# Kernel tuning notes

Measured on AMD Instinct MI355X. Metric: run time of the kernel, lower is better.

Reference implementation:

```python
import jax, jax.numpy as jnp
import numpy as np

B, T = 64, 500
N_EX, N_SK = 10000, 100
H, K = 128, 32


def setup_inputs() -> dict:
    key = jax.random.key(0)
    ks = jax.random.split(key, 32)
    g = lambda i, shape, s=0.05: (jax.random.normal(ks[i], shape, dtype=jnp.float32) * s)
    inp = {
        's_data': jax.random.randint(ks[0], (B, T), 0, N_SK),
        'a_data': jax.random.randint(ks[1], (B, T), 0, 2),
        'e_data': jax.random.randint(ks[2], (B, T), 0, N_EX),
        'at_data': jax.random.randint(ks[3], (B, T), 0, 100),
        'q_matrix': (jax.random.uniform(ks[4], (N_EX + 1, N_SK + 1)) < 0.05).astype(jnp.float32),
        's_embed_w': g(5, (N_SK + 1, H)),
        'a_embed_w': g(6, (2, H)),
        'e_embed_w': g(7, (N_EX + 1, H)),
        'W1': g(8, (H, 2 * H)), 'b1': jnp.zeros((H,), jnp.float32),
        'W2': g(9, (H, 3 * H)), 'b2': jnp.zeros((H,), jnp.float32),
        'W3': g(10, (H, 2 * H)), 'b3': jnp.zeros((H,), jnp.float32),
        'key_matrix': g(11, (K, H)),
        'gru_w_ih': g(12, (3 * H, H)), 'gru_w_hh': g(13, (3 * H, H)),
        'gru_b_ih': jnp.zeros((3 * H,), jnp.float32), 'gru_b_hh': jnp.zeros((3 * H,), jnp.float32),
        'Wg': g(14, (H, 2 * H)), 'bg': jnp.zeros((H,), jnp.float32),
        'Wgg': g(15, (H, 2 * H)), 'bgg': jnp.zeros((H,), jnp.float32),
        'Wf': g(16, (H, 2 * H)), 'bf': jnp.zeros((H,), jnp.float32),
        'Wp': g(17, (1, 3 * H)), 'bp': jnp.zeros((1,), jnp.float32),
        'Wp1': g(18, (1, 3 * H)), 'bp1': jnp.zeros((1,), jnp.float32),
        'h0': g(19, (H,)),           # xavier init of GRU initial state (shared across batch)
        'm0': g(20, (K, H)),         # xavier init of memory h_pre (shared across batch)
    }
    return inp


def reference(s_data, a_data, e_data, at_data, q_matrix, s_embed_w, a_embed_w, e_embed_w,
              W1, b1, W2, b2, W3, b3, key_matrix, gru_w_ih, gru_w_hh, gru_b_ih, gru_b_hh,
              Wg, bg, Wgg, bgg, Wf, bf, Wp, bp, Wp1, bp1, h0, m0):
    # eval mode: dropout = identity
    Bv, Tv = a_data.shape
    lin = lambda x, W, b: x @ W.T + b
    # ---- embedding (n_exercise > 0 branch) ----
    rel = q_matrix[e_data]                              # [B,T,S+1]
    ssum = rel.sum(-1, keepdims=True)
    ssum = jnp.where(ssum == 0, 1.0, ssum)
    s_emb = jnp.einsum('bts,sh->bth', rel, s_embed_w) / ssum
    e_emb = e_embed_w[e_data]
    a_emb = a_embed_w[a_data]
    se_data = jax.nn.relu(lin(jnp.concatenate([s_emb, e_emb], -1), W1, b1))
    se_learning = jax.nn.relu(lin(jnp.concatenate([s_emb, e_emb, a_emb], -1), W2, b2))
    e_learning = jax.nn.relu(lin(jnp.concatenate([e_emb, a_emb], -1), W3, b3))
    # ---- GRU over e_learning ----
    gx = jnp.einsum('bth,gh->btg', e_learning, gru_w_ih) + gru_b_ih  # [B,T,3H]
    def gru_step(h, gxt):
        gh = h @ gru_w_hh.T + gru_b_hh
        xr, xz, xn = jnp.split(gxt, 3, -1)
        hr, hz, hn = jnp.split(gh, 3, -1)
        r = jax.nn.sigmoid(xr + hr)
        z = jax.nn.sigmoid(xz + hz)
        n = jnp.tanh(xn + r * hn)
        hn2 = (1 - z) * n + z * h
        return hn2, hn2
    _, gru_out = jax.lax.scan(gru_step, jnp.broadcast_to(h0, (Bv, h0.shape[0])), jnp.swapaxes(gx, 0, 1))
    out = jnp.swapaxes(gru_out, 0, 1)[:, :-1]           # [B,T-1,H]
    # ---- key-value memory scan ----
    Wall = jnp.einsum('bth,kh->btk', se_data, key_matrix)  # attention weights (unnormalized)
    h_pre0 = jnp.broadcast_to(m0, (Bv,) + m0.shape)        # [B,K,H]
    ht0 = jnp.einsum('bk,bkh->bh', Wall[:, 0], h_pre0)
    xs = (jnp.swapaxes(Wall[:, :-1], 0, 1),
          jnp.swapaxes(Wall[:, 1:], 0, 1),
          jnp.swapaxes(se_learning[:, :-1], 0, 1))
    def step(carry, x):
        h_pre, ht_pre = carry
        w, w_next, learning = x
        hl = jnp.concatenate([ht_pre, learning], -1)
        gain = jnp.tanh(hl @ Wg.T + bg)
        gate = jax.nn.sigmoid(hl @ Wgg.T + bgg)
        LG = gate * gain                                  # [B,H]
        LG_t = w[:, :, None] * LG[:, None, :]             # [B,K,H] write
        gam = jax.nn.sigmoid(jnp.concatenate([h_pre, jnp.broadcast_to(LG[:, None, :], h_pre.shape)], -1) @ Wf.T + bf)
        h = gam * h_pre + LG_t
        ht = jnp.einsum('bk,bkh->bh', w_next, h)          # read at t+1
        return (h, ht), ht
    _, hts = jax.lax.scan(step, (h_pre0, ht0), xs)
    out1 = jnp.swapaxes(hts, 0, 1)                        # [B,T-1,H]
    sg = jax.lax.stop_gradient
    res = jax.nn.sigmoid(jnp.concatenate([out, sg(out1), e_emb[:, 1:]], -1) @ Wp.T + bp)[..., 0]
    res1 = jax.nn.sigmoid(jnp.concatenate([sg(out), out1, se_data[:, 1:]], -1) @ Wp1.T + bp1)[..., 0]
    pred = jnp.zeros((Bv, Tv), res.dtype).at[:, 1:].set(res * res1)
    return pred
```

## Files before the change

kernel.cpp:

```cpp
#include <hip/hip_runtime.h>

#define TT 500
typedef __attribute__((ext_vector_type(8))) short short8v;
typedef __attribute__((ext_vector_type(4))) short short4v;
typedef __attribute__((ext_vector_type(4))) float float4v;
typedef unsigned short ushort;

__device__ __forceinline__ ushort f2bf(float f) {
  union { float f; unsigned u; } v; v.f = f;
  unsigned r = v.u + 0x7FFFu + ((v.u >> 16) & 1u);
  return (ushort)(r >> 16);
}
__device__ __forceinline__ ushort f2bfr(float f) {
  union { float f; unsigned u; } v; v.f = f;
  return (ushort)((v.u + 0x8000u) >> 16);
}
__device__ __forceinline__ float bf2f(ushort u) {
  union { unsigned u; float f; } v; v.u = ((unsigned)u) << 16;
  return v.f;
}
__device__ __forceinline__ float sigm(float x) {
  return __builtin_amdgcn_rcpf(1.f + __builtin_amdgcn_exp2f(-1.44269504088896341f * x));
}
__device__ __forceinline__ float tanh_f(float x) {
  return 1.f - 2.f * __builtin_amdgcn_rcpf(1.f + __builtin_amdgcn_exp2f(2.88539008177792682f * x));
}
__device__ __forceinline__ void bar_lds() {
  asm volatile("s_waitcnt lgkmcnt(0)\ns_barrier" ::: "memory");
}
template <int CTRL>
__device__ __forceinline__ float dppadd(float v) {
  int a = __builtin_amdgcn_update_dpp(0, __builtin_bit_cast(int, v), CTRL, 0xF, 0xF, true);
  return v + __builtin_bit_cast(float, a);
}
__device__ __forceinline__ float rsum16(float v) {
  v = dppadd<0xB1>(v);
  v = dppadd<0x4E>(v);
  v = dppadd<0x141>(v);
  v = dppadd<0x140>(v);
  return v;
}
#define MFMA __builtin_amdgcn_mfma_f32_16x16x32_bf16

__global__ __launch_bounds__(256) void conv_k(
    const float* __restrict__ W1, const float* __restrict__ W2,
    const float* __restrict__ W3, const float* __restrict__ Wih,
    const float* __restrict__ key, const float* __restrict__ Wg,
    const float* __restrict__ Wgg, ushort* __restrict__ wts)
{
  int idx = blockIdx.x * 256 + threadIdx.x;
  if (idx >= 200704) return;
  float v;
  if (idx < 32768)       v = W1[idx];
  else if (idx < 81920)  v = W2[idx - 32768];
  else if (idx < 114688) v = W3[idx - 81920];
  else if (idx < 163840) v = Wih[idx - 114688];
  else if (idx < 167936) v = key[idx - 163840];
  else {
    int j = idx - 167936, o = j >> 7, k = j & 127;
    v = (o < 128) ? Wg[o * 256 + 128 + k] : Wgg[(o - 128) * 256 + 128 + k];
  }
  wts[idx] = f2bf(v);
}

__global__ __launch_bounds__(256) void ph_gather_k(
    const int* __restrict__ a_data, const int* __restrict__ e_data,
    const float* __restrict__ qm, const float* __restrict__ semb,
    const float* __restrict__ aemb, const float* __restrict__ eemb,
    ushort* __restrict__ Xg)
{
  const int tid = threadIdx.x;
  const int tok = tid >> 4, l16 = tid & 15;
  const int gt = blockIdx.x * 16 + tok;
  const int e = e_data[gt], a = a_data[gt];
  const float* qrow = qm + (size_t)e * 101;
  float qv[7];
#pragma unroll
  for (int i = 0; i < 7; ++i) {
    int s = l16 + 16 * i;
    qv[i] = (s < 101) ? qrow[s] : 0.f;
  }
  const float* sbase = semb + l16 * 8;
  float4v acc0 = {0,0,0,0}, acc1 = {0,0,0,0};
  float cnt = 0.f;
#pragma unroll
  for (int i = 0; i < 7; ++i) {
    unsigned long long bal = __ballot(qv[i] != 0.f);
    unsigned m = (unsigned)((bal >> (tid & 48)) & 0xFFFFull);
    cnt += (float)__popc(m);
    while (m) {
      int s = 16 * i + __builtin_ctz(m);
      m &= m - 1;
      acc0 += *(const float4v*)(sbase + s * 128);
      acc1 += *(const float4v*)(sbase + s * 128 + 4);
    }
  }
  float inv = 1.f / fmaxf(cnt, 1.f);
  ushort* xr = Xg + (size_t)gt * 384 + l16 * 8;
  const float* ee = eemb + (size_t)e * 128 + l16 * 8;
  const float* ae = aemb + a * 128 + l16 * 8;
  short4v p0, p1;
#pragma unroll
  for (int r = 0; r < 4; ++r) { p0[r] = (short)f2bf(acc0[r] * inv); p1[r] = (short)f2bf(acc1[r] * inv); }
  *(short4v*)(xr) = p0;
  *(short4v*)(xr + 4) = p1;
#pragma unroll
  for (int r = 0; r < 8; ++r) { xr[128 + r] = f2bf(ee[r]); xr[256 + r] = f2bf(ae[r]); }
}

#define XS 424
#define SS 648

__global__ __launch_bounds__(256, 2) void ph_gemm_k(
    const float* __restrict__ b1, const float* __restrict__ b2,
    const float* __restrict__ b3, const float* __restrict__ bih,
    const float* __restrict__ bg, const float* __restrict__ bgg,
    const float* __restrict__ Wp, const float* __restrict__ bp,
    const float* __restrict__ Wp1, const float* __restrict__ bp1,
    const ushort* __restrict__ wts,
    ushort* __restrict__ gxb, ushort* __restrict__ xgx,
    float* __restrict__ wallb, float* __restrict__ c1b, float* __restrict__ c2b)
{
  __shared__ __align__(16) ushort sbuf[27136];
  ushort* Xl = sbuf;
  ushort* Yl = sbuf + 13568;
  ushort* St = sbuf;
  const int tid = threadIdx.x;
  const int b = blockIdx.x >> 4, chunk = blockIdx.x & 15;
  const int t0 = chunk * 32;
  const int NT = (TT - t0 < 32) ? (TT - t0) : 32;
  const ushort* w1b  = wts;
  const ushort* w2b  = wts + 32768;
  const ushort* w3b  = wts + 81920;
  const ushort* wihb = wts + 114688;
  const ushort* keyb = wts + 163840;
  const ushort* wgb  = wts + 167936;

#pragma unroll
  for (int pass = 0; pass < 2; ++pass) {
    const int tok = (tid >> 4) + pass * 16, sg = tid & 15;
    const int tsrc = (tok < NT) ? tok : (NT - 1);
    size_t gt = (size_t)b * TT + t0 + tsrc;
#pragma unroll
    for (int p = 0; p < 3; ++p)
      *(short8v*)(Xl + tok * XS + sg * 24 + p * 8) = *(const short8v*)(gxb + gt * 384 + sg * 24 + p * 8);
  }
  __syncthreads();

  const int w = tid >> 6, l = tid & 63, jj = l & 15, seg = l >> 4;

  if (tid < 32) {
    int tau = tid;
    if (tau < NT) {
      const ushort* xr = Xl + tau * XS + 128;
      const float* wv = Wp + 256;
      float a0 = bp[0], a1 = 0.f, a2 = 0.f, a3 = 0.f;
      for (int j = 0; j < 128; j += 4) {
        a0 = fmaf(wv[j],     bf2f(xr[j]),     a0);
        a1 = fmaf(wv[j + 1], bf2f(xr[j + 1]), a1);
        a2 = fmaf(wv[j + 2], bf2f(xr[j + 2]), a2);
        a3 = fmaf(wv[j + 3], bf2f(xr[j + 3]), a3);
      }
      c1b[b * TT + t0 + tau] = (a0 + a1) + (a2 + a3);
    }
  }

  short8v axA[12], axB[12];
#pragma unroll
  for (int i = 0; i < 12; ++i) {
    axA[i] = *(short8v*)(Xl + jj * XS + i * 32 + seg * 8);
    axB[i] = *(short8v*)(Xl + (16 + jj) * XS + i * 32 + seg * 8);
  }

  for (int T = w; T < 24; T += 4) {
    float4v dA = {0,0,0,0}, dB = {0,0,0,0};
    float bv;
    if (T < 8) {
      const ushort* Bp = w1b + (T * 16 + jj) * 256 + seg * 8;
      bv = b1[T * 16 + jj];
#pragma unroll
      for (int k = 0; k < 8; ++k) {
        short8v bw = *(const short8v*)(Bp + k * 32);
        dA = MFMA(axA[k], bw, dA, 0, 0, 0);
        dB = MFMA(axB[k], bw, dB, 0, 0, 0);
      }
    } else if (T < 16) {
      const ushort* Bp = w2b + ((T - 8) * 16 + jj) * 384 + seg * 8;
      bv = b2[(T - 8) * 16 + jj];
#pragma unroll
      for (int k = 0; k < 12; ++k) {
        short8v bw = *(const short8v*)(Bp + k * 32);
        dA = MFMA(axA[k], bw, dA, 0, 0, 0);
        dB = MFMA(axB[k], bw, dB, 0, 0, 0);
      }
    } else {
      const ushort* Bp = w3b + ((T - 16) * 16 + jj) * 256 + seg * 8;
      bv = b3[(T - 16) * 16 + jj];
#pragma unroll
      for (int k = 0; k < 8; ++k) {
        short8v bw = *(const short8v*)(Bp + k * 32);
        dA = MFMA(axA[4 + k], bw, dA, 0, 0, 0);
        dB = MFMA(axB[4 + k], bw, dB, 0, 0, 0);
      }
    }
#pragma unroll
    for (int r = 0; r < 4; ++r) {
      float yA = dA[r] + bv, yB = dB[r] + bv;
      Yl[(seg * 4 + r) * XS + T * 16 + jj]      = f2bf(yA > 0.f ? yA : 0.f);
      Yl[(16 + seg * 4 + r) * XS + T * 16 + jj] = f2bf(yB > 0.f ? yB : 0.f);
    }
  }
  __syncthreads();

  short8v ayA[12], ayB[12];
#pragma unroll
  for (int i = 0; i < 12; ++i) {
    ayA[i] = *(short8v*)(Yl + jj * XS + i * 32 + seg * 8);
    ayB[i] = *(short8v*)(Yl + (16 + jj) * XS + i * 32 + seg * 8);
  }

  if (tid >= 32 && tid < 64) {
    int tau = tid - 32;
    if (tau < NT) {
      const ushort* xr = Yl + tau * XS;
      const float* wv = Wp1 + 256;
      float a0 = bp1[0], a1 = 0.f, a2 = 0.f, a3 = 0.f;
      for (int j = 0; j < 128; j += 4) {
        a0 = fmaf(wv[j],     bf2f(xr[j]),     a0);
        a1 = fmaf(wv[j + 1], bf2f(xr[j + 1]), a1);
        a2 = fmaf(wv[j + 2], bf2f(xr[j + 2]), a2);
        a3 = fmaf(wv[j + 3], bf2f(xr[j + 3]), a3);
      }
      c2b[b * TT + t0 + tau] = (a0 + a1) + (a2 + a3);
    }
  }
  __syncthreads();

  for (int T = w; T < 42; T += 4) {
    const ushort* Bp; int ai;
    if (T < 24)      { Bp = wihb + (T * 16 + jj) * 128 + seg * 8;        ai = 8; }
    else if (T < 40) { Bp = wgb  + ((T - 24) * 16 + jj) * 128 + seg * 8; ai = 4; }
    else             { Bp = keyb + ((T - 40) * 16 + jj) * 128 + seg * 8; ai = 0; }
    float4v dA = {0,0,0,0}, dB = {0,0,0,0};
#pragma unroll
    for (int k = 0; k < 4; ++k) {
      short8v bw = *(const short8v*)(Bp + k * 32);
      dA = MFMA(ayA[ai + k], bw, dA, 0, 0, 0);
      dB = MFMA(ayB[ai + k], bw, dB, 0, 0, 0);
    }
    if (T < 40) {
      float bv = (T < 24) ? bih[T * 16 + jj]
               : (T < 32) ? bg[(T - 24) * 16 + jj] : bgg[(T - 32) * 16 + jj];
      int col = (T < 24) ? (T * 16 + jj) : (384 + (T - 24) * 16 + jj);
#pragma unroll
      for (int r = 0; r < 4; ++r) {
        St[(seg * 4 + r) * SS + col]      = f2bf(dA[r] + bv);
        St[(16 + seg * 4 + r) * SS + col] = f2bf(dB[r] + bv);
      }
    } else {
#pragma unroll
      for (int r = 0; r < 4; ++r) {
        int tokA = seg * 4 + r, tokB = 16 + seg * 4 + r;
        if (tokA < NT)
          wallb[((size_t)(b * TT + t0 + tokA)) * 32 + (T - 40) * 16 + jj] = dA[r];
        if (tokB < NT)
          wallb[((size_t)(b * TT + t0 + tokB)) * 32 + (T - 40) * 16 + jj] = dB[r];
      }
    }
  }
  __syncthreads();

#pragma unroll
  for (int pass = 0; pass < 2; ++pass) {
    const int tok = (tid >> 4) + pass * 16, sg = tid & 15;
    if (tok < NT) {
      size_t gt = (size_t)b * TT + t0 + tok;
#pragma unroll
      for (int p = 0; p < 3; ++p)
        *(short8v*)(gxb + gt * 384 + sg * 24 + p * 8) = *(short8v*)(St + tok * SS + sg * 24 + p * 8);
#pragma unroll
      for (int p = 0; p < 2; ++p)
        *(short8v*)(xgx + gt * 256 + sg * 16 + p * 8) = *(short8v*)(St + tok * SS + 384 + sg * 16 + p * 8);
    }
  }
}

__global__ __launch_bounds__(512) void scan_k(
    const float* __restrict__ Wf, const float* __restrict__ bf_,
    const float* __restrict__ Wg, const float* __restrict__ Wgg,
    const float* __restrict__ Whh, const float* __restrict__ bhh,
    const float* __restrict__ h0v, const float* __restrict__ m0,
    const ushort* __restrict__ gxb, const ushort* __restrict__ xgx,
    const float* __restrict__ wallb,
    ushort* __restrict__ htsm, ushort* __restrict__ htsg)
{
  const int tid = threadIdx.x;
  const int w = tid >> 6, l = tid & 63, jj = l & 15, seg = l >> 4;
  const int n0 = w * 16 + seg * 4;

  if (blockIdx.x < 64) {
    const int b = blockIdx.x;
    __shared__ __align__(16) ushort h_bf[32 * 128];
    __shared__ __align__(16) ushort htb[128];
    __shared__ __align__(16) ushort LGb[128];

    short8v afrA[4], aggA[4], aggB[4], alg[4];
#pragma unroll
    for (int ks = 0; ks < 4; ++ks) {
      const float* sA = Wf  + (w * 16 + jj) * 256 + ks * 32 + seg * 8;
      const float* sB = Wg  + (w * 16 + jj) * 256 + ks * 32 + seg * 8;
      const float* sC = Wgg + (w * 16 + jj) * 256 + ks * 32 + seg * 8;
      const float* sD = Wf  + (w * 16 + jj) * 256 + 128 + ks * 32 + seg * 8;
      short8v a, bb, c, d;
#pragma unroll
      for (int j = 0; j < 8; ++j) {
        a[j] = (short)f2bf(sA[j]); bb[j] = (short)f2bf(sB[j]);
        c[j] = (short)f2bf(sC[j]); d[j] = (short)f2bf(sD[j]);
      }
      afrA[ks] = a; aggA[ks] = bb; aggB[ks] = c; alg[ks] = d;
    }
    const float4v bf4 = *(const float4v*)(bf_ + n0);

    float hreg[2][4];
#pragma unroll
    for (int nt = 0; nt < 2; ++nt) {
      int k = nt * 16 + jj;
      float4v m = *(const float4v*)(m0 + k * 128 + n0);
#pragma unroll
      for (int r = 0; r < 4; ++r) hreg[nt][r] = m[r];
      int p = ((n0 >> 3) + k) & 15;
      short4v pk;
#pragma unroll
      for (int r = 0; r < 4; ++r) pk[r] = (short)f2bf(hreg[nt][r]);
      *(short4v*)(h_bf + k * 128 + p * 8 + (n0 & 7)) = pk;
    }
    const float* wl = wallb + (size_t)b * TT * 32;
    const ushort* xgp = xgx + (size_t)b * TT * 256;
    float wv0 = wl[jj], wv1 = wl[16 + jj];
    float wn0 = wl[32 + jj], wn1 = wl[48 + jj];
    short4v xcg  = *(const short4v*)(xgp + n0);
    short4v xcgg = *(const short4v*)(xgp + 128 + n0);
    short4v xng  = *(const short4v*)(xgp + 256 + n0);
    short4v xngg = *(const short4v*)(xgp + 384 + n0);
    {
      float4v htp;
#pragma unroll
      for (int r = 0; r < 4; ++r)
        htp[r] = rsum16(wv0 * hreg[0][r] + wv1 * hreg[1][r]);
      if (jj == 0) {
        short4v hp;
#pragma unroll
        for (int r = 0; r < 4; ++r) hp[r] = (short)f2bf(htp[r]);
        *(short4v*)(htb + n0) = hp;
      }
    }
    __syncthreads();

    for (int t = 0; t < TT - 1; ++t) {
      int tw = (t + 2 <= TT - 1) ? (t + 2) : (TT - 1);
      float wf0 = wl[tw * 32 + jj], wf1 = wl[tw * 32 + 16 + jj];
      short4v xfg  = *(const short4v*)(xgp + (size_t)tw * 256 + n0);
      short4v xfgg = *(const short4v*)(xgp + (size_t)tw * 256 + 128 + n0);

      short8v hb[4];
#pragma unroll
      for (int ks = 0; ks < 4; ++ks)
        hb[ks] = *(short8v*)(htb + ks * 32 + seg * 8);

      float4v xg4, xgg4;
#pragma unroll
      for (int r = 0; r < 4; ++r) { xg4[r] = bf2f((ushort)xcg[r]); xgg4[r] = bf2f((ushort)xcgg[r]); }
      float4v dg0 = xg4, dg1 = {0,0,0,0}, gg0 = xgg4, gg1 = {0,0,0,0};
      dg0 = MFMA(aggA[0], hb[0], dg0, 0, 0, 0);
      dg0 = MFMA(aggA[1], hb[1], dg0, 0, 0, 0);
      dg1 = MFMA(aggA[2], hb[2], dg1, 0, 0, 0);
      dg1 = MFMA(aggA[3], hb[3], dg1, 0, 0, 0);
      gg0 = MFMA(aggB[0], hb[0], gg0, 0, 0, 0);
      gg0 = MFMA(aggB[1], hb[1], gg0, 0, 0, 0);
      gg1 = MFMA(aggB[2], hb[2], gg1, 0, 0, 0);
      gg1 = MFMA(aggB[3], hb[3], gg1, 0, 0, 0);

      float lgv[4];
#pragma unroll
      for (int r = 0; r < 4; ++r)
        lgv[r] = tanh_f(dg0[r] + dg1[r]) * sigm(gg0[r] + gg1[r]);
      if (jj == 0) {
        short4v lp;
#pragma unroll
        for (int r = 0; r < 4; ++r) lp[r] = (short)f2bfr(lgv[r]);
        *(short4v*)(LGb + n0) = lp;
      }

      short8v bv0[4], bv1[4];
#pragma unroll
      for (int ks = 0; ks < 4; ++ks) {
        int g = ks * 4 + seg;
        bv0[ks] = *(short8v*)(h_bf + jj * 128 + ((g + jj) & 15) * 8);
        bv1[ks] = *(short8v*)(h_bf + (16 + jj) * 128 + ((g + 16 + jj) & 15) * 8);
      }
      float4v a0A = {0,0,0,0}, a0B = {0,0,0,0}, a1A = {0,0,0,0}, a1B = {0,0,0,0};
      a0A = MFMA(afrA[0], bv0[0], a0A, 0, 0, 0);
      a0A = MFMA(afrA[1], bv0[1], a0A, 0, 0, 0);
      a0B = MFMA(afrA[2], bv0[2], a0B, 0, 0, 0);
      a0B = MFMA(afrA[3], bv0[3], a0B, 0, 0, 0);
      a1A = MFMA(afrA[0], bv1[0], a1A, 0, 0, 0);
      a1A = MFMA(afrA[1], bv1[1], a1A, 0, 0, 0);
      a1B = MFMA(afrA[2], bv1[2], a1B, 0, 0, 0);
      a1B = MFMA(afrA[3], bv1[3], a1B, 0, 0, 0);
      bar_lds();

      short8v lb[4];
#pragma unroll
      for (int ks = 0; ks < 4; ++ks)
        lb[ks] = *(short8v*)(LGb + ks * 32 + seg * 8);
      float4v dl0 = bf4, dl1 = {0,0,0,0};
      dl0 = MFMA(alg[0], lb[0], dl0, 0, 0, 0);
      dl0 = MFMA(alg[1], lb[1], dl0, 0, 0, 0);
      dl1 = MFMA(alg[2], lb[2], dl1, 0, 0, 0);
      dl1 = MFMA(alg[3], lb[3], dl1, 0, 0, 0);

      float4v htp = {0,0,0,0};
#pragma unroll
      for (int nt = 0; nt < 2; ++nt) {
        float wvv = nt ? wv1 : wv0;
        float wnn = nt ? wn1 : wn0;
#pragma unroll
        for (int r = 0; r < 4; ++r) {
          float a = nt ? (a1A[r] + a1B[r]) : (a0A[r] + a0B[r]);
          float gam = sigm(a + dl0[r] + dl1[r]);
          float hn = fmaf(gam, hreg[nt][r], wvv * lgv[r]);
          hreg[nt][r] = hn;
          htp[r] = fmaf(wnn, hn, htp[r]);
        }
        int k = nt * 16 + jj;
        int p = ((n0 >> 3) + k) & 15;
        short4v pk;
#pragma unroll
        for (int r = 0; r < 4; ++r) pk[r] = (short)f2bfr(hreg[nt][r]);
        *(short4v*)(h_bf + k * 128 + p * 8 + (n0 & 7)) = pk;
      }
#pragma unroll
      for (int r = 0; r < 4; ++r) htp[r] = rsum16(htp[r]);
      if (jj == 0) {
        short4v hp;
#pragma unroll
        for (int r = 0; r < 4; ++r) hp[r] = (short)f2bfr(htp[r]);
        *(short4v*)(htb + n0) = hp;
        *(short4v*)(htsm + ((size_t)b * TT + t) * 128 + n0) = hp;
      }
      wv0 = wn0; wv1 = wn1; wn0 = wf0; wn1 = wf1;
      xcg = xng; xcgg = xngg; xng = xfg; xngg = xfgg;
      bar_lds();
    }
  } else {
    const int b = blockIdx.x - 64;
    __shared__ __align__(16) ushort hb2[2][128];

    short8v wfr[3][4];
    float4v bfr[3];
#pragma unroll
    for (int i = 0; i < 3; ++i) {
      int Mt = w + i * 8;
#pragma unroll
      for (int ks = 0; ks < 4; ++ks) {
        const float* src = Whh + (Mt * 16 + jj) * 128 + ks * 32 + seg * 8;
        short8v tv;
#pragma unroll
        for (int j = 0; j < 8; ++j) tv[j] = (short)f2bf(src[j]);
        wfr[i][ks] = tv;
      }
      bfr[i] = *(const float4v*)(bhh + Mt * 16 + seg * 4);
    }
    const ushort* gpb = gxb + (size_t)b * TT * 384;
    float4v hj4 = *(const float4v*)(h0v + n0);
    if (jj == 0) {
      short4v hp;
#pragma unroll
      for (int r = 0; r < 4; ++r) hp[r] = (short)f2bf(hj4[r]);
      *(short4v*)(&hb2[0][n0]) = hp;
    }
    short4v xr_c = *(const short4v*)(gpb + n0);
    short4v xz_c = *(const short4v*)(gpb + 128 + n0);
    short4v xn_c = *(const short4v*)(gpb + 256 + n0);
    short4v xr_n = *(const short4v*)(gpb + 384 + n0);
    short4v xz_n = *(const short4v*)(gpb + 512 + n0);
    short4v xn_n = *(const short4v*)(gpb + 640 + n0);
    __syncthreads();

    for (int t = 0; t < TT - 1; ++t) {
      int tf = (t + 2 < TT - 1) ? (t + 2) : (TT - 2);
      const ushort* gf = gpb + (size_t)tf * 384;
      short4v xr_f = *(const short4v*)(gf + n0);
      short4v xz_f = *(const short4v*)(gf + 128 + n0);
      short4v xn_f = *(const short4v*)(gf + 256 + n0);

      const ushort* hsrc = hb2[t & 1];
      short8v bfrg[4];
#pragma unroll
      for (int ks = 0; ks < 4; ++ks)
        bfrg[ks] = *(short8v*)(hsrc + ks * 32 + seg * 8);

      float4v a0A = bfr[0], a1A = bfr[1], a2A = bfr[2];
      float4v a0B = {0,0,0,0}, a1B = {0,0,0,0}, a2B = {0,0,0,0};
      a0A = MFMA(wfr[0][0], bfrg[0], a0A, 0, 0, 0);
      a0A = MFMA(wfr[0][1], bfrg[1], a0A, 0, 0, 0);
      a0B = MFMA(wfr[0][2], bfrg[2], a0B, 0, 0, 0);
      a0B = MFMA(wfr[0][3], bfrg[3], a0B, 0, 0, 0);
      a1A = MFMA(wfr[1][0], bfrg[0], a1A, 0, 0, 0);
      a1A = MFMA(wfr[1][1], bfrg[1], a1A, 0, 0, 0);
      a1B = MFMA(wfr[1][2], bfrg[2], a1B, 0, 0, 0);
      a1B = MFMA(wfr[1][3], bfrg[3], a1B, 0, 0, 0);
      a2A = MFMA(wfr[2][0], bfrg[0], a2A, 0, 0, 0);
      a2A = MFMA(wfr[2][1], bfrg[1], a2A, 0, 0, 0);
      a2B = MFMA(wfr[2][2], bfrg[2], a2B, 0, 0, 0);
      a2B = MFMA(wfr[2][3], bfrg[3], a2B, 0, 0, 0);

      ushort* hdst = (ushort*)hb2[(t + 1) & 1];
      short4v hp;
#pragma unroll
      for (int r = 0; r < 4; ++r) {
        float rr = sigm(bf2f((ushort)xr_c[r]) + a0A[r] + a0B[r]);
        float zz = sigm(bf2f((ushort)xz_c[r]) + a1A[r] + a1B[r]);
        float nn = tanh_f(bf2f((ushort)xn_c[r]) + rr * (a2A[r] + a2B[r]));
        hj4[r] = fmaf(1.f - zz, nn, zz * hj4[r]);
        hp[r] = (short)f2bfr(hj4[r]);
      }
      if (jj == 0) {
        *(short4v*)(hdst + n0) = hp;
        *(short4v*)(htsg + ((size_t)b * TT + t) * 128 + n0) = hp;
      }
      xr_c = xr_n; xz_c = xz_n; xn_c = xn_n;
      xr_n = xr_f; xz_n = xz_f; xn_n = xn_f;
      bar_lds();
    }
  }
}

__global__ __launch_bounds__(256) void combine_k(
    const ushort* __restrict__ htsg, const ushort* __restrict__ htsm,
    const float* __restrict__ c1b, const float* __restrict__ c2b,
    const float* __restrict__ Wp, const float* __restrict__ Wp1,
    float* __restrict__ out)
{
  const int b = blockIdx.x;
  const int wv = threadIdx.x >> 6;
  const int lane = threadIdx.x & 63;
  const float w0 = Wp[lane], w1 = Wp[64 + lane], w2 = Wp[128 + lane], w3 = Wp[192 + lane];
  const float v0 = Wp1[lane], v1 = Wp1[64 + lane], v2 = Wp1[128 + lane], v3 = Wp1[192 + lane];
  if (threadIdx.x == 0) out[(size_t)b * TT] = 0.f;
  for (int tau = wv; tau < TT - 1; tau += 4) {
    size_t base = ((size_t)b * TT + tau) * 128;
    float hg0 = bf2f(htsg[base + lane]), hg1 = bf2f(htsg[base + 64 + lane]);
    float hm0 = bf2f(htsm[base + lane]), hm1 = bf2f(htsm[base + 64 + lane]);
    float qa = hg0 * w0 + hg1 * w1 + hm0 * w2 + hm1 * w3;
    float qb = hg0 * v0 + hg1 * v1 + hm0 * v2 + hm1 * v3;
#pragma unroll
    for (int m = 1; m < 64; m <<= 1) {
      qa += __shfl_xor(qa, m, 64);
      qb += __shfl_xor(qb, m, 64);
    }
    if (lane == 0) {
      size_t idx = (size_t)b * TT + tau + 1;
      out[idx] = sigm(qa + c1b[idx]) * sigm(qb + c2b[idx]);
    }
  }
}

extern "C" void kernel_launch(void* const* d_in, const int* in_sizes, int n_in,
                              void* d_out, int out_size, void* d_ws, size_t ws_size,
                              hipStream_t stream) {
  (void)in_sizes; (void)n_in; (void)out_size; (void)ws_size;
  const int* a_data = (const int*)d_in[1];
  const int* e_data = (const int*)d_in[2];
  const float* qm   = (const float*)d_in[4];
  const float* semb = (const float*)d_in[5];
  const float* aemb = (const float*)d_in[6];
  const float* eemb = (const float*)d_in[7];
  const float* W1 = (const float*)d_in[8];   const float* b1 = (const float*)d_in[9];
  const float* W2 = (const float*)d_in[10];  const float* b2 = (const float*)d_in[11];
  const float* W3 = (const float*)d_in[12];  const float* b3 = (const float*)d_in[13];
  const float* key = (const float*)d_in[14];
  const float* Wih = (const float*)d_in[15]; const float* Whh = (const float*)d_in[16];
  const float* bih = (const float*)d_in[17]; const float* bhh = (const float*)d_in[18];
  const float* Wg  = (const float*)d_in[19]; const float* bg  = (const float*)d_in[20];
  const float* Wgg = (const float*)d_in[21]; const float* bgg = (const float*)d_in[22];
  const float* Wf  = (const float*)d_in[23]; const float* bf_ = (const float*)d_in[24];
  const float* Wp  = (const float*)d_in[25]; const float* bp  = (const float*)d_in[26];
  const float* Wp1 = (const float*)d_in[27]; const float* bp1 = (const float*)d_in[28];
  const float* h0v = (const float*)d_in[29]; const float* m0  = (const float*)d_in[30];

  char* ws = (char*)d_ws;
  ushort* gxb  = (ushort*)(ws + 0);
  ushort* xgx  = (ushort*)(ws + 24576000);
  float* wallb = (float*)(ws + 40960000);
  ushort* htsm = (ushort*)(ws + 45056000);
  ushort* htsg = (ushort*)(ws + 53248000);
  float* c1b   = (float*)(ws + 61440000);
  float* c2b   = (float*)(ws + 61568000);
  ushort* wts  = (ushort*)(ws + 61696000);
  float* out = (float*)d_out;

  conv_k<<<dim3(784), dim3(256), 0, stream>>>(W1, W2, W3, Wih, key, Wg, Wgg, wts);
  ph_gather_k<<<dim3(2000), dim3(256), 0, stream>>>(
      a_data, e_data, qm, semb, aemb, eemb, gxb);
  ph_gemm_k<<<dim3(1024), dim3(256), 0, stream>>>(
      b1, b2, b3, bih, bg, bgg, Wp, bp, Wp1, bp1, wts,
      gxb, xgx, wallb, c1b, c2b);
  scan_k<<<dim3(128), dim3(512), 0, stream>>>(
      Wf, bf_, Wg, Wgg, Whh, bhh, h0v, m0, gxb, xgx, wallb, htsm, htsg);
  combine_k<<<dim3(64), dim3(256), 0, stream>>>(
      htsg, htsm, c1b, c2b, Wp, Wp1, out);
}
```

Before: 949.9 us.

## Fuse gather, projection GEMM and scans into one persistent kernel with flags

Merges the gather, projection GEMM and both recurrent scan kernels into a single launch. Blocks 0-127 run the sequential scans and spin on per-(chunk,batch) flags, while the remaining 1024 blocks gather embeddings, run the GEMMs for 32-token chunks, and set a release flag when each chunk is written. The scans can then start before all projections finish, overlapping the serial recurrence with the parallel precompute and removing the launch gaps and the gxb round trip from the gather stage. The risk is that it relies on scan blocks and producer blocks being co-resident and on forward progress, and the producer blocks now use 512 threads with halved per-warp tile loops.

Result: faster. 917.1 us (-3.5%).

```diff
diff --git a/kernel.cpp b/kernel.cpp
--- a/kernel.cpp
+++ b/kernel.cpp
@@ -39,6 +39,11 @@
   v = dppadd<0x141>(v);
   v = dppadd<0x140>(v);
   return v;
+}
+__device__ __forceinline__ void wait_flag(int* f) {
+  while (__hip_atomic_load(f, __ATOMIC_RELAXED, __HIP_MEMORY_SCOPE_AGENT) == 0)
+    __builtin_amdgcn_s_sleep(8);
+  __builtin_amdgcn_fence(__ATOMIC_ACQUIRE, "agent");
 }
 #define MFMA __builtin_amdgcn_mfma_f32_16x16x32_bf16
 
@@ -63,246 +68,38 @@
   wts[idx] = f2bf(v);
 }
 
-__global__ __launch_bounds__(256) void ph_gather_k(
+#define XS 424
+#define SS 648
+
+__global__ __launch_bounds__(512) void mega_k(
     const int* __restrict__ a_data, const int* __restrict__ e_data,
     const float* __restrict__ qm, const float* __restrict__ semb,
     const float* __restrict__ aemb, const float* __restrict__ eemb,
-    ushort* __restrict__ Xg)
-{
-  const int tid = threadIdx.x;
-  const int tok = tid >> 4, l16 = tid & 15;
-  const int gt = blockIdx.x * 16 + tok;
-  const int e = e_data[gt], a = a_data[gt];
-  const float* qrow = qm + (size_t)e * 101;
-  float qv[7];
-#pragma unroll
-  for (int i = 0; i < 7; ++i) {
-    int s = l16 + 16 * i;
-    qv[i] = (s < 101) ? qrow[s] : 0.f;
-  }
-  const float* sbase = semb + l16 * 8;
-  float4v acc0 = {0,0,0,0}, acc1 = {0,0,0,0};
-  float cnt = 0.f;
-#pragma unroll
-  for (int i = 0; i < 7; ++i) {
-    unsigned long long bal = __ballot(qv[i] != 0.f);
-    unsigned m = (unsigned)((bal >> (tid & 48)) & 0xFFFFull);
-    cnt += (float)__popc(m);
-    while (m) {
-      int s = 16 * i + __builtin_ctz(m);
-      m &= m - 1;
-      acc0 += *(const float4v*)(sbase + s * 128);
-      acc1 += *(const float4v*)(sbase + s * 128 + 4);
-    }
-  }
-  float inv = 1.f / fmaxf(cnt, 1.f);
-  ushort* xr = Xg + (size_t)gt * 384 + l16 * 8;
-  const float* ee = eemb + (size_t)e * 128 + l16 * 8;
-  const float* ae = aemb + a * 128 + l16 * 8;
-  short4v p0, p1;
-#pragma unroll
-  for (int r = 0; r < 4; ++r) { p0[r] = (short)f2bf(acc0[r] * inv); p1[r] = (short)f2bf(acc1[r] * inv); }
-  *(short4v*)(xr) = p0;
-  *(short4v*)(xr + 4) = p1;
-#pragma unroll
-  for (int r = 0; r < 8; ++r) { xr[128 + r] = f2bf(ee[r]); xr[256 + r] = f2bf(ae[r]); }
-}
-
-#define XS 424
-#define SS 648
-
-__global__ __launch_bounds__(256, 2) void ph_gemm_k(
     const float* __restrict__ b1, const float* __restrict__ b2,
     const float* __restrict__ b3, const float* __restrict__ bih,
     const float* __restrict__ bg, const float* __restrict__ bgg,
     const float* __restrict__ Wp, const float* __restrict__ bp,
     const float* __restrict__ Wp1, const float* __restrict__ bp1,
     const ushort* __restrict__ wts,
-    ushort* __restrict__ gxb, ushort* __restrict__ xgx,
-    float* __restrict__ wallb, float* __restrict__ c1b, float* __restrict__ c2b)
-{
-  __shared__ __align__(16) ushort sbuf[27136];
-  ushort* Xl = sbuf;
-  ushort* Yl = sbuf + 13568;
-  ushort* St = sbuf;
-  const int tid = threadIdx.x;
-  const int b = blockIdx.x >> 4, chunk = blockIdx.x & 15;
-  const int t0 = chunk * 32;
-  const int NT = (TT - t0 < 32) ? (TT - t0) : 32;
-  const ushort* w1b  = wts;
-  const ushort* w2b  = wts + 32768;
-  const ushort* w3b  = wts + 81920;
-  const ushort* wihb = wts + 114688;
-  const ushort* keyb = wts + 163840;
-  const ushort* wgb  = wts + 167936;
-
-#pragma unroll
-  for (int pass = 0; pass < 2; ++pass) {
-    const int tok = (tid >> 4) + pass * 16, sg = tid & 15;
-    const int tsrc = (tok < NT) ? tok : (NT - 1);
-    size_t gt = (size_t)b * TT + t0 + tsrc;
-#pragma unroll
-    for (int p = 0; p < 3; ++p)
-      *(short8v*)(Xl + tok * XS + sg * 24 + p * 8) = *(const short8v*)(gxb + gt * 384 + sg * 24 + p * 8);
-  }
-  __syncthreads();
-
-  const int w = tid >> 6, l = tid & 63, jj = l & 15, seg = l >> 4;
-
-  if (tid < 32) {
-    int tau = tid;
-    if (tau < NT) {
-      const ushort* xr = Xl + tau * XS + 128;
-      const float* wv = Wp + 256;
-      float a0 = bp[0], a1 = 0.f, a2 = 0.f, a3 = 0.f;
-      for (int j = 0; j < 128; j += 4) {
-        a0 = fmaf(wv[j],     bf2f(xr[j]),     a0);
-        a1 = fmaf(wv[j + 1], bf2f(xr[j + 1]), a1);
-        a2 = fmaf(wv[j + 2], bf2f(xr[j + 2]), a2);
-        a3 = fmaf(wv[j + 3], bf2f(xr[j + 3]), a3);
-      }
-      c1b[b * TT + t0 + tau] = (a0 + a1) + (a2 + a3);
-    }
-  }
-
-  short8v axA[12], axB[12];
-#pragma unroll
-  for (int i = 0; i < 12; ++i) {
-    axA[i] = *(short8v*)(Xl + jj * XS + i * 32 + seg * 8);
-    axB[i] = *(short8v*)(Xl + (16 + jj) * XS + i * 32 + seg * 8);
-  }
-
-  for (int T = w; T < 24; T += 4) {
-    float4v dA = {0,0,0,0}, dB = {0,0,0,0};
-    float bv;
-    if (T < 8) {
-      const ushort* Bp = w1b + (T * 16 + jj) * 256 + seg * 8;
-      bv = b1[T * 16 + jj];
-#pragma unroll
-      for (int k = 0; k < 8; ++k) {
-        short8v bw = *(const short8v*)(Bp + k * 32);
-        dA = MFMA(axA[k], bw, dA, 0, 0, 0);
-        dB = MFMA(axB[k], bw, dB, 0, 0, 0);
-      }
-    } else if (T < 16) {
-      const ushort* Bp = w2b + ((T - 8) * 16 + jj) * 384 + seg * 8;
-      bv = b2[(T - 8) * 16 + jj];
-#pragma unroll
-      for (int k = 0; k < 12; ++k) {
-        short8v bw = *(const short8v*)(Bp + k * 32);
-        dA = MFMA(axA[k], bw, dA, 0, 0, 0);
-        dB = MFMA(axB[k], bw, dB, 0, 0, 0);
-      }
-    } else {
-      const ushort* Bp = w3b + ((T - 16) * 16 + jj) * 256 + seg * 8;
-      bv = b3[(T - 16) * 16 + jj];
-#pragma unroll
-      for (int k = 0; k < 8; ++k) {
-        short8v bw = *(const short8v*)(Bp + k * 32);
-        dA = MFMA(axA[4 + k], bw, dA, 0, 0, 0);
-        dB = MFMA(axB[4 + k], bw, dB, 0, 0, 0);
-      }
-    }
-#pragma unroll
-    for (int r = 0; r < 4; ++r) {
-      float yA = dA[r] + bv, yB = dB[r] + bv;
-      Yl[(seg * 4 + r) * XS + T * 16 + jj]      = f2bf(yA > 0.f ? yA : 0.f);
-      Yl[(16 + seg * 4 + r) * XS + T * 16 + jj] = f2bf(yB > 0.f ? yB : 0.f);
-    }
-  }
-  __syncthreads();
-
-  short8v ayA[12], ayB[12];
-#pragma unroll
-  for (int i = 0; i < 12; ++i) {
-    ayA[i] = *(short8v*)(Yl + jj * XS + i * 32 + seg * 8);
-    ayB[i] = *(short8v*)(Yl + (16 + jj) * XS + i * 32 + seg * 8);
-  }
-
-  if (tid >= 32 && tid < 64) {
-    int tau = tid - 32;
-    if (tau < NT) {
-      const ushort* xr = Yl + tau * XS;
-      const float* wv = Wp1 + 256;
-      float a0 = bp1[0], a1 = 0.f, a2 = 0.f, a3 = 0.f;
-      for (int j = 0; j < 128; j += 4) {
-        a0 = fmaf(wv[j],     bf2f(xr[j]),     a0);
-        a1 = fmaf(wv[j + 1], bf2f(xr[j + 1]), a1);
-        a2 = fmaf(wv[j + 2], bf2f(xr[j + 2]), a2);
-        a3 = fmaf(wv[j + 3], bf2f(xr[j + 3]), a3);
-      }
-      c2b[b * TT + t0 + tau] = (a0 + a1) + (a2 + a3);
-    }
-  }
-  __syncthreads();
-
-  for (int T = w; T < 42; T += 4) {
-    const ushort* Bp; int ai;
-    if (T < 24)      { Bp = wihb + (T * 16 + jj) * 128 + seg * 8;        ai = 8; }
-    else if (T < 40) { Bp = wgb  + ((T - 24) * 16 + jj) * 128 + seg * 8; ai = 4; }
-    else             { Bp = keyb + ((T - 40) * 16 + jj) * 128 + seg * 8; ai = 0; }
-    float4v dA = {0,0,0,0}, dB = {0,0,0,0};
-#pragma unroll
-    for (int k = 0; k < 4; ++k) {
-      short8v bw = *(const short8v*)(Bp + k * 32);
-      dA = MFMA(ayA[ai + k], bw, dA, 0, 0, 0);
-      dB = MFMA(ayB[ai + k], bw, dB, 0, 0, 0);
-    }
-    if (T < 40) {
-      float bv = (T < 24) ? bih[T * 16 + jj]
-               : (T < 32) ? bg[(T - 24) * 16 + jj] : bgg[(T - 32) * 16 + jj];
-      int col = (T < 24) ? (T * 16 + jj) : (384 + (T - 24) * 16 + jj);
-#pragma unroll
-      for (int r = 0; r < 4; ++r) {
-        St[(seg * 4 + r) * SS + col]      = f2bf(dA[r] + bv);
-        St[(16 + seg * 4 + r) * SS + col] = f2bf(dB[r] + bv);
-      }
-    } else {
-#pragma unroll
-      for (int r = 0; r < 4; ++r) {
-        int tokA = seg * 4 + r, tokB = 16 + seg * 4 + r;
-        if (tokA < NT)
-          wallb[((size_t)(b * TT + t0 + tokA)) * 32 + (T - 40) * 16 + jj] = dA[r];
-        if (tokB < NT)
-          wallb[((size_t)(b * TT + t0 + tokB)) * 32 + (T - 40) * 16 + jj] = dB[r];
-      }
-    }
-  }
-  __syncthreads();
-
-#pragma unroll
-  for (int pass = 0; pass < 2; ++pass) {
-    const int tok = (tid >> 4) + pass * 16, sg = tid & 15;
-    if (tok < NT) {
-      size_t gt = (size_t)b * TT + t0 + tok;
-#pragma unroll
-      for (int p = 0; p < 3; ++p)
-        *(short8v*)(gxb + gt * 384 + sg * 24 + p * 8) = *(short8v*)(St + tok * SS + sg * 24 + p * 8);
-#pragma unroll
-      for (int p = 0; p < 2; ++p)
-        *(short8v*)(xgx + gt * 256 + sg * 16 + p * 8) = *(short8v*)(St + tok * SS + 384 + sg * 16 + p * 8);
-    }
-  }
-}
-
-__global__ __launch_bounds__(512) void scan_k(
     const float* __restrict__ Wf, const float* __restrict__ bf_,
     const float* __restrict__ Wg, const float* __restrict__ Wgg,
     const float* __restrict__ Whh, const float* __restrict__ bhh,
     const float* __restrict__ h0v, const float* __restrict__ m0,
-    const ushort* __restrict__ gxb, const ushort* __restrict__ xgx,
-    const float* __restrict__ wallb,
-    ushort* __restrict__ htsm, ushort* __restrict__ htsg)
+    ushort* __restrict__ gxb, ushort* __restrict__ xgx,
+    float* __restrict__ wallb, float* __restrict__ c1b, float* __restrict__ c2b,
+    ushort* __restrict__ htsm, ushort* __restrict__ htsg,
+    int* __restrict__ flags)
 {
+  __shared__ __align__(16) ushort pool[27136];
   const int tid = threadIdx.x;
   const int w = tid >> 6, l = tid & 63, jj = l & 15, seg = l >> 4;
   const int n0 = w * 16 + seg * 4;
 
   if (blockIdx.x < 64) {
     const int b = blockIdx.x;
-    __shared__ __align__(16) ushort h_bf[32 * 128];
-    __shared__ __align__(16) ushort htb[128];
-    __shared__ __align__(16) ushort LGb[128];
+    ushort* h_bf = pool;
+    ushort* htb  = pool + 4096;
+    ushort* LGb  = pool + 4224;
 
     short8v afrA[4], aggA[4], aggB[4], alg[4];
 #pragma unroll
@@ -334,6 +131,7 @@
       for (int r = 0; r < 4; ++r) pk[r] = (short)f2bf(hreg[nt][r]);
       *(short4v*)(h_bf + k * 128 + p * 8 + (n0 & 7)) = pk;
     }
+    wait_flag(flags + b);
     const float* wl = wallb + (size_t)b * TT * 32;
     const ushort* xgp = xgx + (size_t)b * TT * 256;
     float wv0 = wl[jj], wv1 = wl[16 + jj];
@@ -358,6 +156,7 @@
 
     for (int t = 0; t < TT - 1; ++t) {
       int tw = (t + 2 <= TT - 1) ? (t + 2) : (TT - 1);
+      if ((tw & 31) == 0) wait_flag(flags + (tw >> 5) * 64 + b);
       float wf0 = wl[tw * 32 + jj], wf1 = wl[tw * 32 + 16 + jj];
       short4v xfg  = *(const short4v*)(xgp + (size_t)tw * 256 + n0);
       short4v xfgg = *(const short4v*)(xgp + (size_t)tw * 256 + 128 + n0);
@@ -452,9 +251,9 @@
       xcg = xng; xcgg = xngg; xng = xfg; xngg = xfgg;
       bar_lds();
     }
-  } else {
+  } else if (blockIdx.x < 128) {
     const int b = blockIdx.x - 64;
-    __shared__ __align__(16) ushort hb2[2][128];
+    ushort* hb2 = pool;
 
     short8v wfr[3][4];
     float4v bfr[3];
@@ -471,14 +270,15 @@
       }
       bfr[i] = *(const float4v*)(bhh + Mt * 16 + seg * 4);
     }
-    const ushort* gpb = gxb + (size_t)b * TT * 384;
     float4v hj4 = *(const float4v*)(h0v + n0);
     if (jj == 0) {
       short4v hp;
 #pragma unroll
       for (int r = 0; r < 4; ++r) hp[r] = (short)f2bf(hj4[r]);
-      *(short4v*)(&hb2[0][n0]) = hp;
-    }
+      *(short4v*)(hb2 + n0) = hp;
+    }
+    wait_flag(flags + b);
+    const ushort* gpb = gxb + (size_t)b * TT * 384;
     short4v xr_c = *(const short4v*)(gpb + n0);
     short4v xz_c = *(const short4v*)(gpb + 128 + n0);
     short4v xn_c = *(const short4v*)(gpb + 256 + n0);
@@ -489,12 +289,13 @@
 
     for (int t = 0; t < TT - 1; ++t) {
       int tf = (t + 2 < TT - 1) ? (t + 2) : (TT - 2);
+      if ((tf & 31) == 0) wait_flag(flags + (tf >> 5) * 64 + b);
       const ushort* gf = gpb + (size_t)tf * 384;
       short4v xr_f = *(const short4v*)(gf + n0);
       short4v xz_f = *(const short4v*)(gf + 128 + n0);
       short4v xn_f = *(const short4v*)(gf + 256 + n0);
 
-      const ushort* hsrc = hb2[t & 1];
+      const ushort* hsrc = hb2 + (t & 1) * 128;
       short8v bfrg[4];
 #pragma unroll
       for (int ks = 0; ks < 4; ++ks)
@@ -515,7 +316,7 @@
       a2B = MFMA(wfr[2][2], bfrg[2], a2B, 0, 0, 0);
       a2B = MFMA(wfr[2][3], bfrg[3], a2B, 0, 0, 0);
 
-      ushort* hdst = (ushort*)hb2[(t + 1) & 1];
+      ushort* hdst = hb2 + ((t + 1) & 1) * 128;
       short4v hp;
 #pragma unroll
       for (int r = 0; r < 4; ++r) {
@@ -533,6 +334,194 @@
       xr_n = xr_f; xz_n = xz_f; xn_n = xn_f;
       bar_lds();
     }
+  } else {
+    const int gi = blockIdx.x - 128;
+    const int chunk = gi >> 6, b = gi & 63;
+    const int t0 = chunk * 32;
+    const int NT = (TT - t0 < 32) ? (TT - t0) : 32;
+    ushort* Xl = pool;
+    ushort* Yl = pool + 13568;
+    ushort* St = pool;
+    const ushort* w1b  = wts;
+    const ushort* w2b  = wts + 32768;
+    const ushort* w3b  = wts + 81920;
+    const ushort* wihb = wts + 114688;
+    const ushort* keyb = wts + 163840;
+    const ushort* wgb  = wts + 167936;
+
+    {
+      const int tok = tid >> 4, l16 = tid & 15;
+      const int tsrc = (tok < NT) ? tok : (NT - 1);
+      const int gt = b * TT + t0 + tsrc;
+      const int e = e_data[gt], a = a_data[gt];
+      const float* qrow = qm + (size_t)e * 101;
+      float qv[7];
+#pragma unroll
+      for (int i = 0; i < 7; ++i) {
+        int s = l16 + 16 * i;
+        qv[i] = (s < 101) ? qrow[s] : 0.f;
+      }
+      const float* sbase = semb + l16 * 8;
+      float4v acc0 = {0,0,0,0}, acc1 = {0,0,0,0};
+      float cnt = 0.f;
+#pragma unroll
+      for (int i = 0; i < 7; ++i) {
+        unsigned long long bal = __ballot(qv[i] != 0.f);
+        unsigned m = (unsigned)((bal >> (tid & 48)) & 0xFFFFull);
+        cnt += (float)__popc(m);
+        while (m) {
+          int s = 16 * i + __builtin_ctz(m);
+          m &= m - 1;
+          acc0 += *(const float4v*)(sbase + s * 128);
+          acc1 += *(const float4v*)(sbase + s * 128 + 4);
+        }
+      }
+      float inv = 1.f / fmaxf(cnt, 1.f);
+      ushort* xr = Xl + tok * XS + l16 * 8;
+#pragma unroll
+      for (int r = 0; r < 4; ++r) { xr[r] = f2bf(acc0[r] * inv); xr[4 + r] = f2bf(acc1[r] * inv); }
+      const float* ee = eemb + (size_t)e * 128 + l16 * 8;
+      const float* ae = aemb + a * 128 + l16 * 8;
+#pragma unroll
+      for (int r = 0; r < 8; ++r) { xr[128 + r] = f2bf(ee[r]); xr[256 + r] = f2bf(ae[r]); }
+    }
+    __syncthreads();
+
+    if (tid < 32) {
+      int tau = tid;
+      if (tau < NT) {
+        const ushort* xr = Xl + tau * XS + 128;
+        const float* wv = Wp + 256;
+        float a0 = bp[0], a1 = 0.f, a2 = 0.f, a3 = 0.f;
+        for (int j = 0; j < 128; j += 4) {
+          a0 = fmaf(wv[j],     bf2f(xr[j]),     a0);
+          a1 = fmaf(wv[j + 1], bf2f(xr[j + 1]), a1);
+          a2 = fmaf(wv[j + 2], bf2f(xr[j + 2]), a2);
+          a3 = fmaf(wv[j + 3], bf2f(xr[j + 3]), a3);
+        }
+        c1b[b * TT + t0 + tau] = (a0 + a1) + (a2 + a3);
+      }
+    }
+
+    short8v axA[12], axB[12];
+#pragma unroll
+    for (int i = 0; i < 12; ++i) {
+      axA[i] = *(short8v*)(Xl + jj * XS + i * 32 + seg * 8);
+      axB[i] = *(short8v*)(Xl + (16 + jj) * XS + i * 32 + seg * 8);
+    }
+
+    for (int T = w; T < 24; T += 8) {
+      float4v dA = {0,0,0,0}, dB = {0,0,0,0};
+      float bv;
+      if (T < 8) {
+        const ushort* Bp = w1b + (T * 16 + jj) * 256 + seg * 8;
+        bv = b1[T * 16 + jj];
+#pragma unroll
+        for (int k = 0; k < 8; ++k) {
+          short8v bw = *(const short8v*)(Bp + k * 32);
+          dA = MFMA(axA[k], bw, dA, 0, 0, 0);
+          dB = MFMA(axB[k], bw, dB, 0, 0, 0);
+        }
+      } else if (T < 16) {
+        const ushort* Bp = w2b + ((T - 8) * 16 + jj) * 384 + seg * 8;
+        bv = b2[(T - 8) * 16 + jj];
+#pragma unroll
+        for (int k = 0; k < 12; ++k) {
+          short8v bw = *(const short8v*)(Bp + k * 32);
+          dA = MFMA(axA[k], bw, dA, 0, 0, 0);
+          dB = MFMA(axB[k], bw, dB, 0, 0, 0);
+        }
+      } else {
+        const ushort* Bp = w3b + ((T - 16) * 16 + jj) * 256 + seg * 8;
+        bv = b3[(T - 16) * 16 + jj];
+#pragma unroll
+        for (int k = 0; k < 8; ++k) {
+          short8v bw = *(const short8v*)(Bp + k * 32);
+          dA = MFMA(axA[4 + k], bw, dA, 0, 0, 0);
+          dB = MFMA(axB[4 + k], bw, dB, 0, 0, 0);
+        }
+      }
+#pragma unroll
+      for (int r = 0; r < 4; ++r) {
+        float yA = dA[r] + bv, yB = dB[r] + bv;
+        Yl[(seg * 4 + r) * XS + T * 16 + jj]      = f2bf(yA > 0.f ? yA : 0.f);
+        Yl[(16 + seg * 4 + r) * XS + T * 16 + jj] = f2bf(yB > 0.f ? yB : 0.f);
+      }
+    }
+    __syncthreads();
+
+    short8v ayA[12], ayB[12];
+#pragma unroll
+    for (int i = 0; i < 12; ++i) {
+      ayA[i] = *(short8v*)(Yl + jj * XS + i * 32 + seg * 8);
+      ayB[i] = *(short8v*)(Yl + (16 + jj) * XS + i * 32 + seg * 8);
+    }
+    if (tid >= 32 && tid < 64) {
+      int tau = tid - 32;
+      if (tau < NT) {
+        const ushort* xr = Yl + tau * XS;
+        const float* wv = Wp1 + 256;
+        float a0 = bp1[0], a1 = 0.f, a2 = 0.f, a3 = 0.f;
+        for (int j = 0; j < 128; j += 4) {
+          a0 = fmaf(wv[j],     bf2f(xr[j]),     a0);
+          a1 = fmaf(wv[j + 1], bf2f(xr[j + 1]), a1);
+          a2 = fmaf(wv[j + 2], bf2f(xr[j + 2]), a2);
+          a3 = fmaf(wv[j + 3], bf2f(xr[j + 3]), a3);
+        }
+        c2b[b * TT + t0 + tau] = (a0 + a1) + (a2 + a3);
+      }
+    }
+    __syncthreads();
+
+    for (int T = w; T < 42; T += 8) {
+      const ushort* Bp; int ai;
+      if (T < 24)      { Bp = wihb + (T * 16 + jj) * 128 + seg * 8;        ai = 8; }
+      else if (T < 40) { Bp = wgb  + ((T - 24) * 16 + jj) * 128 + seg * 8; ai = 4; }
+      else             { Bp = keyb + ((T - 40) * 16 + jj) * 128 + seg * 8; ai = 0; }
+      float4v dA = {0,0,0,0}, dB = {0,0,0,0};
+#pragma unroll
+      for (int k = 0; k < 4; ++k) {
+        short8v bw = *(const short8v*)(Bp + k * 32);
+        dA = MFMA(ayA[ai + k], bw, dA, 0, 0, 0);
+        dB = MFMA(ayB[ai + k], bw, dB, 0, 0, 0);
+      }
+      if (T < 40) {
+        float bv = (T < 24) ? bih[T * 16 + jj]
+                 : (T < 32) ? bg[(T - 24) * 16 + jj] : bgg[(T - 32) * 16 + jj];
+        int col = (T < 24) ? (T * 16 + jj) : (384 + (T - 24) * 16 + jj);
+#pragma unroll
+        for (int r = 0; r < 4; ++r) {
+          St[(seg * 4 + r) * SS + col]      = f2bf(dA[r] + bv);
+          St[(16 + seg * 4 + r) * SS + col] = f2bf(dB[r] + bv);
+        }
+      } else {
+#pragma unroll
+        for (int r = 0; r < 4; ++r) {
+          int tokA = seg * 4 + r, tokB = 16 + seg * 4 + r;
+          if (tokA < NT)
+            wallb[((size_t)(b * TT + t0 + tokA)) * 32 + (T - 40) * 16 + jj] = dA[r];
+          if (tokB < NT)
+            wallb[((size_t)(b * TT + t0 + tokB)) * 32 + (T - 40) * 16 + jj] = dB[r];
+        }
+      }
+    }
+    __syncthreads();
+
+    {
+      const int tok = tid >> 4, sg = tid & 15;
+      if (tok < NT) {
+        size_t gt = (size_t)b * TT + t0 + tok;
+#pragma unroll
+        for (int p = 0; p < 3; ++p)
+          *(short8v*)(gxb + gt * 384 + sg * 24 + p * 8) = *(short8v*)(St + tok * SS + sg * 24 + p * 8);
+#pragma unroll
+        for (int p = 0; p < 2; ++p)
+          *(short8v*)(xgx + gt * 256 + sg * 16 + p * 8) = *(short8v*)(St + tok * SS + 384 + sg * 16 + p * 8);
+      }
+    }
+    __syncthreads();
+    if (tid == 0)
+      __hip_atomic_store(flags + chunk * 64 + b, 1, __ATOMIC_RELEASE, __HIP_MEMORY_SCOPE_AGENT);
   }
 }
 
@@ -598,16 +587,15 @@
   float* c1b   = (float*)(ws + 61440000);
   float* c2b   = (float*)(ws + 61568000);
   ushort* wts  = (ushort*)(ws + 61696000);
+  int* flags   = (int*)(ws + 62097408);
   float* out = (float*)d_out;
 
+  hipMemsetAsync(flags, 0, 1024 * sizeof(int), stream);
   conv_k<<<dim3(784), dim3(256), 0, stream>>>(W1, W2, W3, Wih, key, Wg, Wgg, wts);
-  ph_gather_k<<<dim3(2000), dim3(256), 0, stream>>>(
-      a_data, e_data, qm, semb, aemb, eemb, gxb);
-  ph_gemm_k<<<dim3(1024), dim3(256), 0, stream>>>(
-      b1, b2, b3, bih, bg, bgg, Wp, bp, Wp1, bp1, wts,
-      gxb, xgx, wallb, c1b, c2b);
-  scan_k<<<dim3(128), dim3(512), 0, stream>>>(
-      Wf, bf_, Wg, Wgg, Whh, bhh, h0v, m0, gxb, xgx, wallb, htsm, htsg);
+  mega_k<<<dim3(1152), dim3(512), 0, stream>>>(
+      a_data, e_data, qm, semb, aemb, eemb, b1, b2, b3, bih, bg, bgg,
+      Wp, bp, Wp1, bp1, wts, Wf, bf_, Wg, Wgg, Whh, bhh, h0v, m0,
+      gxb, xgx, wallb, c1b, c2b, htsm, htsg, flags);
   combine_k<<<dim3(64), dim3(256), 0, stream>>>(
       htsg, htsm, c1b, c2b, Wp, Wp1, out);
 }
```
